# Performance work log

Hardware: AMD Instinct MI355X
Metric: run time of the kernel (lower is better)

Reference implementation:

```python
import jax, jax.numpy as jnp
import numpy as np

# Model dims (match init_kwargs)
D_MODEL = 512
N_LAYERS = 4
N_DIST = 32
N_CAT = 32
LATENT = N_DIST * N_CAT  # 1024
D_INNER = 2 * D_MODEL    # 1024 (mamba expand=2)
D_STATE = 16
DT_RANK = D_MODEL // 16  # 32
K = 4                    # depthwise conv kernel
BATCH, SEQ = 4, 1024


def setup_inputs() -> dict:
    key = jax.random.key(0)
    ks = jax.random.split(key, 12)
    f = lambda k, shape, s=0.02: (jax.random.normal(k, shape, jnp.float32) * s)
    inp = {
        "x": jax.random.normal(ks[0], (BATCH, SEQ, LATENT), jnp.float32),
        "lin1_w": f(ks[1], (LATENT, D_MODEL)),
        "lin1_b": jnp.zeros((D_MODEL,), jnp.float32),
        "norm_w": jnp.ones((N_LAYERS, D_MODEL), jnp.float32),
        "in_w": f(ks[2], (N_LAYERS, D_MODEL, 2 * D_INNER)),
        "conv_w": f(ks[3], (N_LAYERS, D_INNER, K), 0.1),
        "conv_b": jnp.zeros((N_LAYERS, D_INNER), jnp.float32),
        "xproj_w": f(ks[4], (N_LAYERS, D_INNER, DT_RANK + 2 * D_STATE)),
        "dt_w": f(ks[5], (N_LAYERS, DT_RANK, D_INNER)),
        "dt_b": f(ks[6], (N_LAYERS, D_INNER), 0.5),
        "A_log": jnp.log(jnp.broadcast_to(
            jnp.arange(1, D_STATE + 1, dtype=jnp.float32),
            (N_LAYERS, D_INNER, D_STATE))),
        "Dp": jnp.ones((N_LAYERS, D_INNER), jnp.float32),
        "out_w": f(ks[7], (N_LAYERS, D_INNER, D_MODEL)),
        "lin2_w": f(ks[8], (D_MODEL, LATENT)),
        "lin2_b": jnp.zeros((LATENT,), jnp.float32),
    }
    return inp


def _rmsnorm(x, w):
    return x * jax.lax.rsqrt(jnp.mean(x * x, axis=-1, keepdims=True) + 1e-5) * w


def _causal_dwconv(x, w, b):
    # x: (B,S,D), w: (D,K) -> depthwise causal conv1d, left-padded
    S = x.shape[1]
    xp = jnp.pad(x, ((0, 0), (K - 1, 0), (0, 0)))
    y = xp[:, 0:S, :] * w[:, 0]
    for k in range(1, K):
        y = y + xp[:, k:k + S, :] * w[:, k]
    return y + b


def _selective_scan(u, dt, Bm, Cm, A, Dvec):
    # u, dt: (B,S,D); Bm, Cm: (B,S,N); A: (D,N); Dvec: (D,)
    dA = jnp.exp(dt[..., None] * A)                               # (B,S,D,N)
    dBu = dt[..., None] * Bm[:, :, None, :] * u[..., None]        # (B,S,D,N)
    h0 = jnp.zeros((u.shape[0], u.shape[2], A.shape[1]), u.dtype)

    def step(h, inputs):
        dA_t, dBu_t, C_t = inputs
        h = dA_t * h + dBu_t                                       # (B,D,N)
        y = jnp.einsum('bdn,bn->bd', h, C_t)
        return h, y

    _, ys = jax.lax.scan(step, h0,
                         (dA.transpose(1, 0, 2, 3),
                          dBu.transpose(1, 0, 2, 3),
                          Cm.transpose(1, 0, 2)))
    return ys.transpose(1, 0, 2) + u * Dvec                       # (B,S,D)


def reference(x, lin1_w, lin1_b, norm_w, in_w, conv_w, conv_b, xproj_w,
              dt_w, dt_b, A_log, Dp, out_w, lin2_w, lin2_b):
    B, S, _ = x.shape
    h = x @ lin1_w + lin1_b                                       # (B,S,d_model)
    for l in range(N_LAYERS):
        resid = h
        hn = _rmsnorm(h, norm_w[l])
        xz = hn @ in_w[l]                                         # (B,S,2*d_inner)
        xp, z = jnp.split(xz, 2, axis=-1)
        xp = jax.nn.silu(_causal_dwconv(xp, conv_w[l], conv_b[l]))
        dbl = xp @ xproj_w[l]                                     # (B,S,dt_rank+2N)
        dt = jax.nn.softplus(dbl[..., :DT_RANK] @ dt_w[l] + dt_b[l])
        Bm = dbl[..., DT_RANK:DT_RANK + D_STATE]
        Cm = dbl[..., DT_RANK + D_STATE:]
        A = -jnp.exp(A_log[l])                                    # (d_inner, N)
        y = _selective_scan(xp, dt, Bm, Cm, A, Dp[l])
        y = y * jax.nn.silu(z)
        h = resid + y @ out_w[l]
    out = h @ lin2_w + lin2_b                                     # (B,S,latent)
    out = jax.nn.softmax(out.reshape(B, S, N_DIST, N_CAT), axis=-1)
    return out.reshape(B, S, N_DIST * N_CAT)
```

## Files before the change

kernel.cpp:

```cpp
#include <hip/hip_runtime.h>
#include <math.h>

#define D_MODEL 512
#define N_LAYERS 4
#define LATENT 1024
#define D_INNER 1024
#define D_STATE 16
#define DT_RANK 32
#define KCONV 4
#define BATCH 4
#define SEQ 1024
#define NTOK (BATCH * SEQ)
#define PCH 32
#define CLEN 32

typedef __attribute__((ext_vector_type(8))) short short8;
typedef __attribute__((ext_vector_type(4))) float floatx4;
typedef unsigned short ushort_t;

#define WC_VM4   0x0F74
#define WC_VM0   0x0F70
#define WC_LGKM0 0xC07F

__device__ __forceinline__ ushort_t f2bf(float f) {
    union { float f; unsigned u; } v; v.f = f;
    unsigned r = v.u + 0x7FFFu + ((v.u >> 16) & 1u);
    return (ushort_t)(r >> 16);
}
__device__ __forceinline__ float bf2f(ushort_t u) {
    union { unsigned u; float f; } v; v.u = ((unsigned)u) << 16;
    return v.f;
}
__device__ __forceinline__ void gll16(const void* g, void* l) {
    __builtin_amdgcn_global_load_lds(
        (const __attribute__((address_space(1))) void*)g,
        (__attribute__((address_space(3))) void*)l, 16, 0, 0);
}

__global__ __launch_bounds__(256, 3) void gemm_bf16_tile(
    const ushort_t* __restrict__ A, int lda,
    const ushort_t* __restrict__ Bt, int ldb,
    float* __restrict__ C, ushort_t* __restrict__ Cb, int ldc,
    const float* __restrict__ bias,
    int M, int N, int K, int flags)
{
    __shared__ ushort_t As[3][4096];
    __shared__ ushort_t Bs[3][4096];

    const int gx = gridDim.x;
    const int nwg = gx * gridDim.y;
    const int orig = blockIdx.y * gx + blockIdx.x;
    const int qq = nwg >> 3, rr = nwg & 7;
    const int xcd = orig & 7, loc = orig >> 3;
    const int swz = (xcd < rr ? xcd * (qq + 1) : rr * (qq + 1) + (xcd - rr) * qq) + loc;
    const int m0 = (swz / gx) * 64;
    const int n0 = (swz % gx) * 64;

    const int tid = threadIdx.x;
    const int w = tid >> 6;
    const int lane = tid & 63;
    const int quad = lane >> 4;
    const int l16 = lane & 15;
    const int wm = (w & 1) * 32;
    const int wn = (w >> 1) * 32;

    const int srow = tid >> 3;
    const int schunk = ((tid & 7) ^ (srow & 7)) * 8;
    const ushort_t* ga = A + (size_t)(m0 + srow) * lda + schunk;
    const ushort_t* gb = Bt + (size_t)(n0 + srow) * ldb + schunk;
    const int lofs = tid * 8;

    const int swz0 = ((0 * 4 + quad) ^ (l16 & 7)) * 8;
    const int swz1 = ((1 * 4 + quad) ^ (l16 & 7)) * 8;

    floatx4 acc[2][2] = {};
    const int nt = K >> 6;

    #define STAGE(t, b)                                         \
        do {                                                    \
            const ushort_t* pa_ = ga + (t) * 64;                \
            const ushort_t* pb_ = gb + (t) * 64;                \
            gll16(pa_, &As[(b)][lofs]);                         \
            gll16(pa_ + (size_t)32 * lda, &As[(b)][2048 + lofs]); \
            gll16(pb_, &Bs[(b)][lofs]);                         \
            gll16(pb_ + (size_t)32 * ldb, &Bs[(b)][2048 + lofs]); \
        } while (0)

    STAGE(0, 0);
    if (nt > 1) STAGE(1, 1);

    int cur = 0;
    for (int kt = 0; kt < nt; kt++) {
        if (kt + 1 < nt) __builtin_amdgcn_s_waitcnt(WC_VM4);
        else             __builtin_amdgcn_s_waitcnt(WC_VM0);
        __builtin_amdgcn_s_barrier();
        __builtin_amdgcn_sched_barrier(0);

        if (kt + 2 < nt) {
            int nb = cur + 2; if (nb >= 3) nb -= 3;
            STAGE(kt + 2, nb);
        }

        short8 af[2][2], bfr[2][2];
        #pragma unroll
        for (int i = 0; i < 2; i++) {
            const int r = wm + i * 16 + l16;
            af[0][i] = *(const short8*)&As[cur][r * 64 + swz0];
            af[1][i] = *(const short8*)&As[cur][r * 64 + swz1];
        }
        #pragma unroll
        for (int j = 0; j < 2; j++) {
            const int r = wn + j * 16 + l16;
            bfr[0][j] = *(const short8*)&Bs[cur][r * 64 + swz0];
            bfr[1][j] = *(const short8*)&Bs[cur][r * 64 + swz1];
        }
        __builtin_amdgcn_s_waitcnt(WC_LGKM0);
        __builtin_amdgcn_sched_barrier(0);

        #pragma unroll
        for (int ks = 0; ks < 2; ks++)
            #pragma unroll
            for (int i = 0; i < 2; i++)
                #pragma unroll
                for (int j = 0; j < 2; j++)
                    acc[i][j] = __builtin_amdgcn_mfma_f32_16x16x32_bf16(
                        af[ks][i], bfr[ks][j], acc[i][j], 0, 0, 0);

        cur++; if (cur == 3) cur = 0;
    }
    #undef STAGE

    #pragma unroll
    for (int j = 0; j < 2; j++) {
        int n = n0 + wn + j * 16 + l16;
        float bv = (flags & 1) ? bias[n] : 0.f;
        bool do_sp = (flags & 4) && (n < 1024);
        float spb = do_sp ? bias[n] : 0.f;
        #pragma unroll
        for (int i = 0; i < 2; i++) {
            int mrow = m0 + wm + i * 16 + quad * 4;
            #pragma unroll
            for (int rr2 = 0; rr2 < 4; rr2++) {
                size_t idx = (size_t)(mrow + rr2) * ldc + n;
                float v = acc[i][j][rr2] + bv;
                if (do_sp) {
                    v += spb;
                    v = (v > 20.f) ? v : log1pf(__expf(v));
                }
                if (flags & 8) {
                    Cb[idx] = f2bf(v);
                } else {
                    if (flags & 2) v += C[idx];
                    C[idx] = v;
                    if (flags & 16) Cb[idx] = f2bf(v);
                }
            }
        }
    }
}

__global__ __launch_bounds__(256) void build_w2t_kernel(
    const float* __restrict__ dt_w, ushort_t* __restrict__ w2t)
{
    const int idx = blockIdx.x * 256 + threadIdx.x;
    const int k = idx & 63;
    const int n = (idx >> 6) & 1023;
    const int l = idx >> 16;
    ushort_t v = 0;
    if (k < 32)
        v = f2bf(dt_w[((size_t)l * DT_RANK + k) * D_INNER + n]);
    w2t[((size_t)l * 1024 + n) * 64 + k] = v;
}

__global__ __launch_bounds__(256) void transpose_cast_kernel(
    const float* __restrict__ in, ushort_t* __restrict__ out, int K, int N)
{
    __shared__ float tile[32][33];
    const int n0 = blockIdx.x * 32, k0 = blockIdx.y * 32;
    const int tx = threadIdx.x & 31, ty = threadIdx.x >> 5;
    #pragma unroll
    for (int i = 0; i < 4; i++)
        tile[ty + i * 8][tx] = in[(size_t)(k0 + ty + i * 8) * N + n0 + tx];
    __syncthreads();
    #pragma unroll
    for (int i = 0; i < 4; i++)
        out[(size_t)(n0 + ty + i * 8) * K + k0 + tx] = f2bf(tile[tx][ty + i * 8]);
}

__global__ __launch_bounds__(256) void cast_bf16_kernel(
    const float* __restrict__ in, ushort_t* __restrict__ out)
{
    const int i = blockIdx.x * 256 + threadIdx.x;
    out[i] = f2bf(in[i]);
}

__global__ __launch_bounds__(256) void rmsnorm_kernel(
    const float* __restrict__ x, const float* __restrict__ w,
    ushort_t* __restrict__ y)
{
    const int row = blockIdx.x;
    const float* xr = x + (size_t)row * D_MODEL;
    ushort_t* yr = y + (size_t)row * D_MODEL;
    const int tid = threadIdx.x;

    float v0 = xr[tid], v1 = xr[tid + 256];
    float ss = v0 * v0 + v1 * v1;
    #pragma unroll
    for (int off = 32; off > 0; off >>= 1) ss += __shfl_down(ss, off);

    __shared__ float wsum[4];
    __shared__ float scale_s;
    int wid = tid >> 6, lane = tid & 63;
    if (lane == 0) wsum[wid] = ss;
    __syncthreads();
    if (tid == 0) {
        float tot = wsum[0] + wsum[1] + wsum[2] + wsum[3];
        scale_s = 1.0f / sqrtf(tot / (float)D_MODEL + 1e-5f);
    }
    __syncthreads();
    float sc = scale_s;
    yr[tid] = f2bf(v0 * sc * w[tid]);
    yr[tid + 256] = f2bf(v1 * sc * w[tid + 256]);
}

__global__ __launch_bounds__(256) void conv_silu_kernel(
    const ushort_t* __restrict__ xz, const float* __restrict__ w,
    const float* __restrict__ bconv, ushort_t* __restrict__ outb)
{
    const int idx = blockIdx.x * 256 + threadIdx.x;
    const int d = idx & (D_INNER - 1);
    const int t = (idx >> 10) & (SEQ - 1);
    const int row = idx >> 10;
    const ushort_t* base = xz + (size_t)row * 2048 + d;

    float s = 0.f;
    #pragma unroll
    for (int k = 0; k < KCONV; k++) {
        int tt = t + k - (KCONV - 1);
        if (tt >= 0)
            s = fmaf(bf2f(base[(ptrdiff_t)(k - (KCONV - 1)) * 2048]), w[d * KCONV + k], s);
    }
    s += bconv[d];
    float r = s / (1.f + __expf(-s));
    outb[idx] = f2bf(r);
}

__global__ __launch_bounds__(256) void scan_pass1(
    const float* __restrict__ dtb, const float* __restrict__ bc,
    const ushort_t* __restrict__ ub, const float* __restrict__ A_log,
    float* __restrict__ hfin, float* __restrict__ sumdt)
{
    const int tid = threadIdx.x;
    const int b = blockIdx.x >> 7;
    const int p = (blockIdx.x >> 2) & 31;
    const int d = ((blockIdx.x & 3) << 8) + tid;
    const int t0 = p * CLEN;

    float A[D_STATE];
    #pragma unroll
    for (int n = 0; n < D_STATE; n++) A[n] = -expf(A_log[d * D_STATE + n]);

    float h[D_STATE] = {};
    float sdt = 0.f;

    const float* dtp = dtb + ((size_t)b * SEQ + t0) * 1024 + d;
    const float* bp  = bc + ((size_t)b * SEQ + t0) * 64 + 32;
    const ushort_t* up = ub + ((size_t)b * SEQ + t0) * D_INNER + d;

    for (int t = 0; t < CLEN; t++) {
        float dtv = dtp[(size_t)t * 1024];
        float uv  = bf2f(up[(size_t)t * D_INNER]);
        float dtu = dtv * uv;
        sdt += dtv;
        #pragma unroll
        for (int n = 0; n < D_STATE; n++)
            h[n] = fmaf(__expf(dtv * A[n]), h[n], dtu * bp[t * 64 + n]);
    }

    size_t base = (size_t)(b * PCH + p) * D_STATE * D_INNER + d;
    #pragma unroll
    for (int n = 0; n < D_STATE; n++) hfin[base + (size_t)n * D_INNER] = h[n];
    sumdt[(size_t)(b * PCH + p) * D_INNER + d] = sdt;
}

__global__ __launch_bounds__(256) void scan_pass2(
    const float* __restrict__ A_log, const float* __restrict__ sumdt,
    float* __restrict__ hc)
{
    const int tid = threadIdx.x;
    const int b = blockIdx.x >> 6;
    const int n = (blockIdx.x >> 2) & 15;
    const int d = ((blockIdx.x & 3) << 8) + tid;

    const float Aval = -expf(A_log[d * D_STATE + n]);
    float h = 0.f;
    for (int p = 0; p < PCH; p++) {
        size_t idx = ((size_t)(b * PCH + p) * D_STATE + n) * D_INNER + d;
        float fin = hc[idx];
        hc[idx] = h;
        h = fmaf(__expf(Aval * sumdt[(size_t)(b * PCH + p) * D_INNER + d]), h, fin);
    }
}

__global__ __launch_bounds__(256) void scan_pass3(
    const float* __restrict__ dtb, const float* __restrict__ bc,
    const ushort_t* __restrict__ xz, const float* __restrict__ A_log,
    const float* __restrict__ Dp, const float* __restrict__ hstart,
    ushort_t* ub)
{
    const int tid = threadIdx.x;
    const int b = blockIdx.x >> 7;
    const int p = (blockIdx.x >> 2) & 31;
    const int d = ((blockIdx.x & 3) << 8) + tid;
    const int t0 = p * CLEN;

    float A[D_STATE];
    #pragma unroll
    for (int n = 0; n < D_STATE; n++) A[n] = -expf(A_log[d * D_STATE + n]);
    const float Dv = Dp[d];

    float h[D_STATE];
    size_t base = (size_t)(b * PCH + p) * D_STATE * D_INNER + d;
    #pragma unroll
    for (int n = 0; n < D_STATE; n++) h[n] = hstart[base + (size_t)n * D_INNER];

    const float* dtp = dtb + ((size_t)b * SEQ + t0) * 1024 + d;
    const float* bp  = bc + ((size_t)b * SEQ + t0) * 64 + 32;
    const ushort_t* zp = xz + ((size_t)b * SEQ + t0) * 2048 + 1024 + d;
    ushort_t* up = ub + ((size_t)b * SEQ + t0) * D_INNER + d;

    for (int t = 0; t < CLEN; t++) {
        float dtv = dtp[(size_t)t * 1024];
        float uv  = bf2f(up[(size_t)t * D_INNER]);
        float zv  = bf2f(zp[(size_t)t * 2048]);
        float dtu = dtv * uv;
        float y = 0.f;
        #pragma unroll
        for (int n = 0; n < D_STATE; n++) {
            h[n] = fmaf(__expf(dtv * A[n]), h[n], dtu * bp[t * 64 + n]);
            y = fmaf(h[n], bp[t * 64 + 16 + n], y);
        }
        float res = fmaf(uv, Dv, y);
        res *= zv / (1.f + __expf(-zv));
        up[(size_t)t * D_INNER] = f2bf(res);
    }
}

__global__ __launch_bounds__(256) void softmax_kernel(
    const float* __restrict__ in, float* __restrict__ out)
{
    const int idx = blockIdx.x * 256 + threadIdx.x;
    float v = in[idx];
    float m = v;
    #pragma unroll
    for (int off = 16; off > 0; off >>= 1) m = fmaxf(m, __shfl_xor(m, off, 32));
    float e = expf(v - m);
    float s = e;
    #pragma unroll
    for (int off = 16; off > 0; off >>= 1) s += __shfl_xor(s, off, 32);
    out[idx] = e / s;
}

extern "C" void kernel_launch(void* const* d_in, const int* in_sizes, int n_in,
                              void* d_out, int out_size, void* d_ws, size_t ws_size,
                              hipStream_t stream)
{
    const float* x       = (const float*)d_in[0];
    const float* lin1_w  = (const float*)d_in[1];
    const float* lin1_b  = (const float*)d_in[2];
    const float* norm_w  = (const float*)d_in[3];
    const float* in_w    = (const float*)d_in[4];
    const float* conv_w  = (const float*)d_in[5];
    const float* conv_b  = (const float*)d_in[6];
    const float* xproj_w = (const float*)d_in[7];
    const float* dt_w    = (const float*)d_in[8];
    const float* dt_b    = (const float*)d_in[9];
    const float* A_log   = (const float*)d_in[10];
    const float* Dp      = (const float*)d_in[11];
    const float* out_w   = (const float*)d_in[12];
    const float* lin2_w  = (const float*)d_in[13];
    const float* lin2_b  = (const float*)d_in[14];
    float* outp = (float*)d_out;
    (void)ws_size; (void)in_sizes; (void)n_in; (void)out_size;

    float* ws = (float*)d_ws;
    const size_t F1M = 1u << 20;
    float* h     = ws;
    float* dtb   = h + 2 * F1M;
    float* dblr  = dtb + 4 * F1M;
    float* sumdt = dblr + (size_t)NTOK * 64;
    float* hfin  = sumdt + (size_t)BATCH * PCH * D_INNER;
    ushort_t* xzb     = (ushort_t*)(hfin + 2 * F1M);
    ushort_t* hn_bf   = xzb + 8 * F1M;
    ushort_t* xb      = hn_bf + 2 * F1M;
    ushort_t* dblr_bf = xb + 4 * F1M;
    ushort_t* lin1_wt = dblr_bf + (size_t)NTOK * 64;
    ushort_t* in_wt   = lin1_wt + (size_t)512 * 1024;
    ushort_t* out_wt  = in_wt + (size_t)4 * 2048 * 512;
    ushort_t* lin2_wt = out_wt + (size_t)4 * 512 * 1024;
    ushort_t* xw_t    = lin2_wt + (size_t)1024 * 512;
    ushort_t* w2t     = xw_t + (size_t)4 * 64 * 1024;

    dim3 blk(256);

    transpose_cast_kernel<<<dim3(512 / 32, 1024 / 32), blk, 0, stream>>>(
        lin1_w, lin1_wt, LATENT, D_MODEL);
    for (int l = 0; l < N_LAYERS; l++) {
        transpose_cast_kernel<<<dim3(2048 / 32, 512 / 32), blk, 0, stream>>>(
            in_w + (size_t)l * 512 * 2048, in_wt + (size_t)l * 2048 * 512, 512, 2048);
        transpose_cast_kernel<<<dim3(512 / 32, 1024 / 32), blk, 0, stream>>>(
            out_w + (size_t)l * 1024 * 512, out_wt + (size_t)l * 512 * 1024, 1024, 512);
        transpose_cast_kernel<<<dim3(64 / 32, 1024 / 32), blk, 0, stream>>>(
            xproj_w + (size_t)l * D_INNER * 64, xw_t + (size_t)l * 64 * 1024, 1024, 64);
    }
    transpose_cast_kernel<<<dim3(1024 / 32, 512 / 32), blk, 0, stream>>>(
        lin2_w, lin2_wt, D_MODEL, LATENT);
    build_w2t_kernel<<<dim3((N_LAYERS * 1024 * 64) / 256), blk, 0, stream>>>(
        dt_w, w2t);

    cast_bf16_kernel<<<dim3((NTOK * LATENT) / 256), blk, 0, stream>>>(x, xb);

    gemm_bf16_tile<<<dim3(D_MODEL / 64, NTOK / 64), blk, 0, stream>>>(
        xb, LATENT, lin1_wt, LATENT, h, nullptr, D_MODEL, lin1_b,
        NTOK, D_MODEL, LATENT, 1);

    for (int l = 0; l < N_LAYERS; l++) {
        const float* nw = norm_w + (size_t)l * D_MODEL;
        const float* cw = conv_w + (size_t)l * D_INNER * KCONV;
        const float* cb = conv_b + (size_t)l * D_INNER;
        const float* db = dt_b + (size_t)l * D_INNER;
        const float* al = A_log + (size_t)l * D_INNER * D_STATE;
        const float* dp = Dp + (size_t)l * D_INNER;
        const ushort_t* iwt = in_wt + (size_t)l * 2048 * 512;
        const ushort_t* owt = out_wt + (size_t)l * 512 * 1024;
        const ushort_t* xwt = xw_t + (size_t)l * 64 * 1024;
        const ushort_t* w2  = w2t + (size_t)l * 1024 * 64;

        rmsnorm_kernel<<<dim3(NTOK), blk, 0, stream>>>(h, nw, hn_bf);

        gemm_bf16_tile<<<dim3(2048 / 64, NTOK / 64), blk, 0, stream>>>(
            hn_bf, D_MODEL, iwt, D_MODEL, nullptr, xzb, 2048, nullptr,
            NTOK, 2048, D_MODEL, 8);

        conv_silu_kernel<<<dim3((NTOK * D_INNER) / 256), blk, 0, stream>>>(
            xzb, cw, cb, xb);

        gemm_bf16_tile<<<dim3(64 / 64, NTOK / 64), blk, 0, stream>>>(
            xb, D_INNER, xwt, D_INNER, dblr, dblr_bf, 64, nullptr,
            NTOK, 64, D_INNER, 16);

        gemm_bf16_tile<<<dim3(1024 / 64, NTOK / 64), blk, 0, stream>>>(
            dblr_bf, 64, w2, 64, dtb, nullptr, 1024, db,
            NTOK, 1024, 64, 4);

        scan_pass1<<<dim3(BATCH * PCH * (D_INNER / 256)), blk, 0, stream>>>(
            dtb, dblr, xb, al, hfin, sumdt);
        scan_pass2<<<dim3(BATCH * D_STATE * (D_INNER / 256)), blk, 0, stream>>>(
            al, sumdt, hfin);
        scan_pass3<<<dim3(BATCH * PCH * (D_INNER / 256)), blk, 0, stream>>>(
            dtb, dblr, xzb, al, dp, hfin, xb);

        gemm_bf16_tile<<<dim3(D_MODEL / 64, NTOK / 64), blk, 0, stream>>>(
            xb, D_INNER, owt, D_INNER, h, nullptr, D_MODEL, nullptr,
            NTOK, D_MODEL, D_INNER, 2);
    }

    cast_bf16_kernel<<<dim3((NTOK * D_MODEL) / 256), blk, 0, stream>>>(h, xb);
    gemm_bf16_tile<<<dim3(LATENT / 64, NTOK / 64), blk, 0, stream>>>(
        xb, D_MODEL, lin2_wt, D_MODEL, dtb, nullptr, LATENT, lin2_b,
        NTOK, LATENT, D_MODEL, 1);
    softmax_kernel<<<dim3((NTOK * LATENT) / 256), blk, 0, stream>>>(dtb, outp);
}
```

Baseline: 756.8 us.

## Split-K the x_proj GEMM with a reduction kernel and batch weight transposes

Replaces the narrow N=64 x_proj GEMM, which launched only 64 blocks, with a split-K kernel over 4 K-slices (256 blocks) that writes partial sums, followed by a reduce kernel that sums them and writes both fp32 and bf16 outputs. Weight transpose launches are merged into per-tensor batched launches using blockIdx.z, and scan_pass2 preloads its per-chunk inputs into registers before the serial recurrence. The split-K path costs extra partial-sum traffic and one more launch per layer in exchange for more parallelism.

New measurement: 720.9 us. 1.05x faster.

```diff
diff --git a/kernel.cpp b/kernel.cpp
--- a/kernel.cpp
+++ b/kernel.cpp
@@ -152,11 +152,121 @@
                 } else {
                     if (flags & 2) v += C[idx];
                     C[idx] = v;
-                    if (flags & 16) Cb[idx] = f2bf(v);
                 }
             }
         }
     }
+}
+
+__global__ __launch_bounds__(256, 3) void gemm_stepA(
+    const ushort_t* __restrict__ A,
+    const ushort_t* __restrict__ Bt,
+    float* __restrict__ Cpart)
+{
+    __shared__ ushort_t As[3][4096];
+    __shared__ ushort_t Bs[3][4096];
+
+    const int kq = blockIdx.x;
+    const int m0 = blockIdx.y * 64;
+    const int k0 = kq * 256;
+
+    const int tid = threadIdx.x;
+    const int w = tid >> 6;
+    const int lane = tid & 63;
+    const int quad = lane >> 4;
+    const int l16 = lane & 15;
+    const int wm = (w & 1) * 32;
+    const int wn = (w >> 1) * 32;
+
+    const int srow = tid >> 3;
+    const int schunk = ((tid & 7) ^ (srow & 7)) * 8;
+    const ushort_t* ga = A + (size_t)(m0 + srow) * 1024 + k0 + schunk;
+    const ushort_t* gb = Bt + (size_t)srow * 1024 + k0 + schunk;
+    const int lofs = tid * 8;
+
+    const int swz0 = ((0 * 4 + quad) ^ (l16 & 7)) * 8;
+    const int swz1 = ((1 * 4 + quad) ^ (l16 & 7)) * 8;
+
+    floatx4 acc[2][2] = {};
+    const int nt = 4;
+
+    #define STAGE(t, b)                                            \
+        do {                                                       \
+            const ushort_t* pa_ = ga + (t) * 64;                   \
+            const ushort_t* pb_ = gb + (t) * 64;                   \
+            gll16(pa_, &As[(b)][lofs]);                            \
+            gll16(pa_ + (size_t)32 * 1024, &As[(b)][2048 + lofs]); \
+            gll16(pb_, &Bs[(b)][lofs]);                            \
+            gll16(pb_ + (size_t)32 * 1024, &Bs[(b)][2048 + lofs]); \
+        } while (0)
+
+    STAGE(0, 0);
+    STAGE(1, 1);
+
+    int cur = 0;
+    for (int kt = 0; kt < nt; kt++) {
+        if (kt + 1 < nt) __builtin_amdgcn_s_waitcnt(WC_VM4);
+        else             __builtin_amdgcn_s_waitcnt(WC_VM0);
+        __builtin_amdgcn_s_barrier();
+        __builtin_amdgcn_sched_barrier(0);
+
+        if (kt + 2 < nt) {
+            int nb = cur + 2; if (nb >= 3) nb -= 3;
+            STAGE(kt + 2, nb);
+        }
+
+        short8 af[2][2], bfr[2][2];
+        #pragma unroll
+        for (int i = 0; i < 2; i++) {
+            const int r = wm + i * 16 + l16;
+            af[0][i] = *(const short8*)&As[cur][r * 64 + swz0];
+            af[1][i] = *(const short8*)&As[cur][r * 64 + swz1];
+        }
+        #pragma unroll
+        for (int j = 0; j < 2; j++) {
+            const int r = wn + j * 16 + l16;
+            bfr[0][j] = *(const short8*)&Bs[cur][r * 64 + swz0];
+            bfr[1][j] = *(const short8*)&Bs[cur][r * 64 + swz1];
+        }
+        __builtin_amdgcn_s_waitcnt(WC_LGKM0);
+        __builtin_amdgcn_sched_barrier(0);
+
+        #pragma unroll
+        for (int ks = 0; ks < 2; ks++)
+            #pragma unroll
+            for (int i = 0; i < 2; i++)
+                #pragma unroll
+                for (int j = 0; j < 2; j++)
+                    acc[i][j] = __builtin_amdgcn_mfma_f32_16x16x32_bf16(
+                        af[ks][i], bfr[ks][j], acc[i][j], 0, 0, 0);
+
+        cur++; if (cur == 3) cur = 0;
+    }
+    #undef STAGE
+
+    float* Cp = Cpart + (size_t)kq * NTOK * 64;
+    #pragma unroll
+    for (int j = 0; j < 2; j++) {
+        int n = wn + j * 16 + l16;
+        #pragma unroll
+        for (int i = 0; i < 2; i++) {
+            int mrow = m0 + wm + i * 16 + quad * 4;
+            #pragma unroll
+            for (int rr2 = 0; rr2 < 4; rr2++)
+                Cp[(size_t)(mrow + rr2) * 64 + n] = acc[i][j][rr2];
+        }
+    }
+}
+
+__global__ __launch_bounds__(256) void reduce_dblr(
+    const float* __restrict__ part, float* __restrict__ dblr,
+    ushort_t* __restrict__ dblr_bf)
+{
+    const int i = blockIdx.x * 256 + threadIdx.x;
+    const size_t st = (size_t)NTOK * 64;
+    float s = part[i] + part[i + st] + part[i + 2 * st] + part[i + 3 * st];
+    dblr[i] = s;
+    dblr_bf[i] = f2bf(s);
 }
 
 __global__ __launch_bounds__(256) void build_w2t_kernel(
@@ -172,9 +282,12 @@
     w2t[((size_t)l * 1024 + n) * 64 + k] = v;
 }
 
-__global__ __launch_bounds__(256) void transpose_cast_kernel(
-    const float* __restrict__ in, ushort_t* __restrict__ out, int K, int N)
-{
+__global__ __launch_bounds__(256) void transpose_cast_b(
+    const float* __restrict__ in0, ushort_t* __restrict__ out0, int K, int N,
+    size_t in_ls, size_t out_ls)
+{
+    const float* in = in0 + (size_t)blockIdx.z * in_ls;
+    ushort_t* out = out0 + (size_t)blockIdx.z * out_ls;
     __shared__ float tile[32][33];
     const int n0 = blockIdx.x * 32, k0 = blockIdx.y * 32;
     const int tx = threadIdx.x & 31, ty = threadIdx.x >> 5;
@@ -293,12 +406,18 @@
     const int d = ((blockIdx.x & 3) << 8) + tid;
 
     const float Aval = -expf(A_log[d * D_STATE + n]);
+
+    float fin[PCH], sd[PCH];
+    #pragma unroll
+    for (int p = 0; p < PCH; p++) {
+        fin[p] = hc[((size_t)(b * PCH + p) * D_STATE + n) * D_INNER + d];
+        sd[p]  = sumdt[(size_t)(b * PCH + p) * D_INNER + d];
+    }
     float h = 0.f;
+    #pragma unroll
     for (int p = 0; p < PCH; p++) {
-        size_t idx = ((size_t)(b * PCH + p) * D_STATE + n) * D_INNER + d;
-        float fin = hc[idx];
-        hc[idx] = h;
-        h = fmaf(__expf(Aval * sumdt[(size_t)(b * PCH + p) * D_INNER + d]), h, fin);
+        hc[((size_t)(b * PCH + p) * D_STATE + n) * D_INNER + d] = h;
+        h = fmaf(__expf(Aval * sd[p]), h, fin[p]);
     }
 }
 
@@ -388,7 +507,8 @@
     float* h     = ws;
     float* dtb   = h + 2 * F1M;
     float* dblr  = dtb + 4 * F1M;
-    float* sumdt = dblr + (size_t)NTOK * 64;
+    float* dpart = dblr + (size_t)NTOK * 64;
+    float* sumdt = dpart + (size_t)4 * NTOK * 64;
     float* hfin  = sumdt + (size_t)BATCH * PCH * D_INNER;
     ushort_t* xzb     = (ushort_t*)(hfin + 2 * F1M);
     ushort_t* hn_bf   = xzb + 8 * F1M;
@@ -403,18 +523,16 @@
 
     dim3 blk(256);
 
-    transpose_cast_kernel<<<dim3(512 / 32, 1024 / 32), blk, 0, stream>>>(
-        lin1_w, lin1_wt, LATENT, D_MODEL);
-    for (int l = 0; l < N_LAYERS; l++) {
-        transpose_cast_kernel<<<dim3(2048 / 32, 512 / 32), blk, 0, stream>>>(
-            in_w + (size_t)l * 512 * 2048, in_wt + (size_t)l * 2048 * 512, 512, 2048);
-        transpose_cast_kernel<<<dim3(512 / 32, 1024 / 32), blk, 0, stream>>>(
-            out_w + (size_t)l * 1024 * 512, out_wt + (size_t)l * 512 * 1024, 1024, 512);
-        transpose_cast_kernel<<<dim3(64 / 32, 1024 / 32), blk, 0, stream>>>(
-            xproj_w + (size_t)l * D_INNER * 64, xw_t + (size_t)l * 64 * 1024, 1024, 64);
-    }
-    transpose_cast_kernel<<<dim3(1024 / 32, 512 / 32), blk, 0, stream>>>(
-        lin2_w, lin2_wt, D_MODEL, LATENT);
+    transpose_cast_b<<<dim3(512 / 32, 1024 / 32, 1), blk, 0, stream>>>(
+        lin1_w, lin1_wt, LATENT, D_MODEL, 0, 0);
+    transpose_cast_b<<<dim3(2048 / 32, 512 / 32, N_LAYERS), blk, 0, stream>>>(
+        in_w, in_wt, 512, 2048, (size_t)512 * 2048, (size_t)2048 * 512);
+    transpose_cast_b<<<dim3(512 / 32, 1024 / 32, N_LAYERS), blk, 0, stream>>>(
+        out_w, out_wt, 1024, 512, (size_t)1024 * 512, (size_t)512 * 1024);
+    transpose_cast_b<<<dim3(64 / 32, 1024 / 32, N_LAYERS), blk, 0, stream>>>(
+        xproj_w, xw_t, 1024, 64, (size_t)1024 * 64, (size_t)64 * 1024);
+    transpose_cast_b<<<dim3(1024 / 32, 512 / 32, 1), blk, 0, stream>>>(
+        lin2_w, lin2_wt, D_MODEL, LATENT, 0, 0);
     build_w2t_kernel<<<dim3((N_LAYERS * 1024 * 64) / 256), blk, 0, stream>>>(
         dt_w, w2t);
 
@@ -445,9 +563,9 @@
         conv_silu_kernel<<<dim3((NTOK * D_INNER) / 256), blk, 0, stream>>>(
             xzb, cw, cb, xb);
 
-        gemm_bf16_tile<<<dim3(64 / 64, NTOK / 64), blk, 0, stream>>>(
-            xb, D_INNER, xwt, D_INNER, dblr, dblr_bf, 64, nullptr,
-            NTOK, 64, D_INNER, 16);
+        gemm_stepA<<<dim3(4, NTOK / 64), blk, 0, stream>>>(xb, xwt, dpart);
+        reduce_dblr<<<dim3((NTOK * 64) / 256), blk, 0, stream>>>(
+            dpart, dblr, dblr_bf);
 
         gemm_bf16_tile<<<dim3(1024 / 64, NTOK / 64), blk, 0, stream>>>(
             dblr_bf, 64, w2, 64, dtb, nullptr, 1024, db,
```
